# Performance work log

Hardware: AMD Instinct MI355X
Metric: run time of the kernel (lower is better)

## Reference

```python
import jax, jax.numpy as jnp
import numpy as np


def setup_inputs() -> dict:
    key = jax.random.key(0)
    k_x, k_q, k_k, k_v = jax.random.split(key, 4)
    B, S, D = 8, 1024, 768
    H, DH = 12, 64
    scale = 1.0 / np.sqrt(D)
    return {
        "x": jax.random.normal(k_x, (B, S, D), dtype=jnp.float32),
        "Wq": jax.random.normal(k_q, (H, D, DH), dtype=jnp.float32) * scale,
        "Wk": jax.random.normal(k_k, (H, D, DH), dtype=jnp.float32) * scale,
        "Wv": jax.random.normal(k_v, (H, D, DH), dtype=jnp.float32) * scale,
    }


def reference(x, Wq, Wk, Wv):
    # x: [B, S, D]; Wq/Wk/Wv: [H, D, DH] (per-head Linear weights, no bias)
    B, S, D = x.shape
    H, _, DH = Wq.shape
    q = jnp.einsum("bsd,hde->bhse", x, Wq)  # [B,H,S,DH]
    k = jnp.einsum("bsd,hde->bhse", x, Wk)
    v = jnp.einsum("bsd,hde->bhse", x, Wv)
    scores = jnp.einsum("bhse,bhte->bhst", q, k) / jnp.sqrt(jnp.float32(DH))
    causal = jnp.tril(jnp.ones((S, S), dtype=bool))  # keep lower triangle
    scores = jnp.where(causal, scores, -jnp.inf)
    attn = jax.nn.softmax(scores, axis=-1)  # dropout = 0.0 -> identity
    ctx = jnp.einsum("bhst,bhte->bhse", attn, v)  # [B,H,S,DH]
    # concat heads on last dim: [B,S,H*DH]
    return ctx.transpose(0, 2, 1, 3).reshape(B, S, H * DH)
```

## Files before the change

kernel.cpp:

```cpp
#include <hip/hip_runtime.h>


#define Bq 8
#define Sq 1024
#define Dq 768
#define Hq 12
#define DHq 64

typedef _Float16 f16;
typedef f16 f16x8 __attribute__((ext_vector_type(8)));
typedef float f32x4 __attribute__((ext_vector_type(4)));

#define MFMA16(a, b, c) __builtin_amdgcn_mfma_f32_16x16x32_f16(a, b, c, 0, 0, 0)

#define QSCL 0.1803368801111244f

#if __has_builtin(__builtin_amdgcn_exp2f)
#define EXP2(x) __builtin_amdgcn_exp2f(x)
#else
#define EXP2(x) exp2f(x)
#endif

__device__ __forceinline__ void gload16(const f16* g, f16* l) {
  __builtin_amdgcn_global_load_lds(
      (const __attribute__((address_space(1))) void*)g,
      (__attribute__((address_space(3))) void*)l, 16, 0, 0);
}

__global__ __launch_bounds__(256) void cvt_x_kernel(const float* __restrict__ x,
                                                    f16* __restrict__ xh) {
  int i = blockIdx.x * 256 + threadIdx.x;
  const float4* src = reinterpret_cast<const float4*>(x) + i * 2;
  float4 a = src[0], b = src[1];
  f16x8 o;
  o[0] = (f16)a.x; o[1] = (f16)a.y; o[2] = (f16)a.z; o[3] = (f16)a.w;
  o[4] = (f16)b.x; o[5] = (f16)b.y; o[6] = (f16)b.z; o[7] = (f16)b.w;
  *reinterpret_cast<f16x8*>(xh + i * 8) = o;
}

__global__ __launch_bounds__(256) void cvt_w_kernel(const float* __restrict__ Wq,
                                                    const float* __restrict__ Wk,
                                                    const float* __restrict__ Wv,
                                                    f16* __restrict__ WT) {
  __shared__ float tile[64][65];
  const int kt = blockIdx.x, h = blockIdx.y, w = blockIdx.z;
  const float* W = (w == 0) ? Wq : (w == 1) ? Wk : Wv;
  const int t = threadIdx.x;
  const int c0 = t & 63, r4 = t >> 6;
#pragma unroll
  for (int i = 0; i < 16; i++) {
    int kr = i * 4 + r4;
    tile[kr][c0] = W[((size_t)h * Dq + kt * 64 + kr) * DHq + c0];
  }
  __syncthreads();
#pragma unroll
  for (int i = 0; i < 16; i++) {
    int e2 = i * 4 + r4;
    WT[((size_t)(w * Hq + h) * DHq + e2) * Dq + kt * 64 + c0] = (f16)tile[c0][e2];
  }
}

__global__ __launch_bounds__(256) void proj_kernel(const f16* __restrict__ xh,
                                                   const f16* __restrict__ WT,
                                                   f16* __restrict__ Q,
                                                   f16* __restrict__ K,
                                                   f16* __restrict__ Vt) {
  __shared__ __align__(1024) f16 smem[30720];

  const int L = blockIdx.x;
  const int j = L >> 3;
  const int mt = (L & 7) + 8 * (j & 7);
  const int h = j >> 3;
  const int row0 = mt * 128;
  const int t = threadIdx.x;
  const int wv = t >> 6;
  const int lane = t & 63;
  const int g = lane >> 4;
  const int ql = lane & 15;
  const int wvm = wv >> 1, wvn = wv & 1;

  const int lr = lane >> 2;
  const int scg = (lane & 3) ^ ((lane >> 3) & 3);

  const f16* xsrc = xh + (size_t)row0 * Dq;
  const f16* wsrc = WT + (size_t)h * DHq * Dq;

  const f16* gA0 = xsrc + (size_t)(wv * 32 + lr) * Dq + scg * 8;
  const f16* gA1 = gA0 + (size_t)16 * Dq;
  const int n0 = wv * 48 + lr, n1 = n0 + 16, n2 = n0 + 32;
  const f16* gB0 = wsrc + ((size_t)(n0 >> 6) * Hq * DHq + (n0 & 63)) * Dq + scg * 8;
  const f16* gB1 = wsrc + ((size_t)(n1 >> 6) * Hq * DHq + (n1 & 63)) * Dq + scg * 8;
  const f16* gB2 = wsrc + ((size_t)(n2 >> 6) * Hq * DHq + (n2 & 63)) * Dq + scg * 8;

  f32x4 acc[4][6] = {};

#define PROJ_STAGE(buf)                                              \
  do {                                                               \
    f16* sA_ = smem + (buf) * 4096 + wv * 1024;                      \
    f16* sB_ = smem + 12288 + (buf) * 6144 + wv * 1536;              \
    gload16(gA0, sA_); gload16(gA1, sA_ + 512);                      \
    gload16(gB0, sB_); gload16(gB1, sB_ + 512);                      \
    gload16(gB2, sB_ + 1024);                                        \
    gA0 += 32; gA1 += 32; gB0 += 32; gB1 += 32; gB2 += 32;           \
  } while (0)

  PROJ_STAGE(0);
  PROJ_STAGE(1);

  const int rq = (g ^ ((ql >> 1) & 3)) * 8;
  const f16* rA = smem + (wvm * 64 + ql) * 32 + rq;
  const f16* rB = smem + 12288 + (wvn * 96 + ql) * 32 + rq;

#pragma unroll
  for (int step = 0; step < 24; step++) {
    if (step < 23) asm volatile("s_waitcnt vmcnt(5) lgkmcnt(0)" ::: "memory");
    else           asm volatile("s_waitcnt vmcnt(0) lgkmcnt(0)" ::: "memory");
    __builtin_amdgcn_s_barrier();
    __builtin_amdgcn_sched_barrier(0);
    if (step < 22) PROJ_STAGE((step + 2) % 3);
    const int cur = step % 3;
    f16x8 af[4], bf[6];
#pragma unroll
    for (int mf = 0; mf < 4; mf++)
      af[mf] = *reinterpret_cast<const f16x8*>(rA + cur * 4096 + mf * 512);
#pragma unroll
    for (int nf = 0; nf < 6; nf++)
      bf[nf] = *reinterpret_cast<const f16x8*>(rB + cur * 6144 + nf * 512);
    __builtin_amdgcn_s_setprio(1);
#pragma unroll
    for (int mf = 0; mf < 4; mf++)
#pragma unroll
      for (int nf = 0; nf < 6; nf++)
        acc[mf][nf] = MFMA16(af[mf], bf[nf], acc[mf][nf]);
    __builtin_amdgcn_s_setprio(0);
  }
#undef PROJ_STAGE
  __syncthreads();

  const int b = row0 >> 10;
  const int s0 = row0 & 1023;
  const size_t base_sd = ((size_t)(b * Hq + h) * Sq) * DHq;

#pragma unroll
  for (int nf = 0; nf < 6; nf++) {
    const int c = wvn * 96 + nf * 16 + ql;
    const int w = c >> 6;
    if (w < 2) {
      f16* dst = (w == 0 ? Q : K);
      const float scl = (w == 0) ? QSCL : 1.0f;
      const int e = c & 63;
#pragma unroll
      for (int mf = 0; mf < 4; mf++) {
        const int sr = wvm * 64 + mf * 16 + g * 4;
#pragma unroll
        for (int r = 0; r < 4; r++)
          dst[base_sd + (size_t)(s0 + sr + r) * DHq + e] = (f16)(acc[mf][nf][r] * scl);
      }
    }
  }

  f16* vbuf = smem;
#pragma unroll
  for (int nf = 2; nf < 6; nf++) {
    if (wvn == 1) {
      const int e = (96 + nf * 16 + ql) & 63;
#pragma unroll
      for (int mf = 0; mf < 4; mf++) {
        const int sr = wvm * 64 + mf * 16 + g * 4;
        union { f16 hh[4]; uint2 u; } z;
#pragma unroll
        for (int r = 0; r < 4; r++) z.hh[r] = (f16)acc[mf][nf][r];
        *reinterpret_cast<uint2*>(&vbuf[e * 136 + sr]) = z.u;
      }
    }
  }
  __syncthreads();
#pragma unroll
  for (int i = 0; i < 4; i++) {
    int c = t + 256 * i;
    int e = c >> 4, p = (c & 15) * 8;
    *reinterpret_cast<uint4*>(Vt + base_sd + (size_t)e * Sq + s0 + p) =
        *reinterpret_cast<const uint4*>(vbuf + e * 136 + p);
  }
}

__global__ __launch_bounds__(256) void attn_kernel(const f16* __restrict__ Q,
                                                   const f16* __restrict__ K,
                                                   const f16* __restrict__ Vt,
                                                   float* __restrict__ out) {
  __shared__ __align__(16) f16 k_lds[2][64][72];
  __shared__ __align__(16) f16 vt_lds[2][64][72];
  __shared__ __align__(16) f16 p_lds[4][16][72];

  const int L = blockIdx.x;
  const int i = L >> 3;
  const int bh = (L & 7) * Hq + (i % Hq);
  const int p = 7 - (i / Hq);
  const int MT = 2 * p + 1;
  const int t = threadIdx.x;
  const int wv = t >> 6;
  const int lane = t & 63;
  const int g = lane >> 4;
  const int ql = lane & 15;

  const f16* Qb = Q + (size_t)bh * Sq * DHq;
  const f16* Kb = K + (size_t)bh * Sq * DHq;
  const f16* Vtb = Vt + (size_t)bh * DHq * Sq;
  const int b = bh / Hq, h = bh % Hq;

  const int r0 = t >> 3;
  const int p0 = (t & 7) * 8;

  const int qg0 = 2 * p * 64 + wv * 16 + ql;
  const int qg1 = qg0 + 64;
  f16x8 qf[2][2];
  qf[0][0] = *reinterpret_cast<const f16x8*>(Qb + (size_t)qg0 * DHq + g * 8);
  qf[0][1] = *reinterpret_cast<const f16x8*>(Qb + (size_t)qg0 * DHq + 32 + g * 8);
  qf[1][0] = *reinterpret_cast<const f16x8*>(Qb + (size_t)qg1 * DHq + g * 8);
  qf[1][1] = *reinterpret_cast<const f16x8*>(Qb + (size_t)qg1 * DHq + 32 + g * 8);

  f32x4 o_acc[2][4] = {};
  float m_r[2] = { -__builtin_inff(), -__builtin_inff() };
  float l_r[2] = { 0.f, 0.f };

  uint4 kreg0, kreg1, vreg0, vreg1;
  kreg0 = *reinterpret_cast<const uint4*>(Kb + (size_t)r0 * DHq + p0);
  kreg1 = *reinterpret_cast<const uint4*>(Kb + (size_t)(32 + r0) * DHq + p0);
  vreg0 = *reinterpret_cast<const uint4*>(Vtb + (size_t)r0 * Sq + p0);
  vreg1 = *reinterpret_cast<const uint4*>(Vtb + (size_t)(32 + r0) * Sq + p0);
  *reinterpret_cast<uint4*>(&k_lds[0][r0][p0]) = kreg0;
  *reinterpret_cast<uint4*>(&k_lds[0][32 + r0][p0]) = kreg1;
  *reinterpret_cast<uint4*>(&vt_lds[0][r0][p0]) = vreg0;
  *reinterpret_cast<uint4*>(&vt_lds[0][32 + r0][p0]) = vreg1;
  kreg0 = *reinterpret_cast<const uint4*>(Kb + (size_t)(64 + r0) * DHq + p0);
  kreg1 = *reinterpret_cast<const uint4*>(Kb + (size_t)(96 + r0) * DHq + p0);
  vreg0 = *reinterpret_cast<const uint4*>(Vtb + (size_t)r0 * Sq + 64 + p0);
  vreg1 = *reinterpret_cast<const uint4*>(Vtb + (size_t)(32 + r0) * Sq + 64 + p0);
  __syncthreads();

  int cur = 0;
  for (int kt = 0; kt <= MT; kt++) {
    if (kt < MT) {
      *reinterpret_cast<uint4*>(&k_lds[cur ^ 1][r0][p0]) = kreg0;
      *reinterpret_cast<uint4*>(&k_lds[cur ^ 1][32 + r0][p0]) = kreg1;
      *reinterpret_cast<uint4*>(&vt_lds[cur ^ 1][r0][p0]) = vreg0;
      *reinterpret_cast<uint4*>(&vt_lds[cur ^ 1][32 + r0][p0]) = vreg1;
      if (kt + 2 <= MT) {
        const int kv0 = (kt + 2) * 64;
        kreg0 = *reinterpret_cast<const uint4*>(Kb + (size_t)(kv0 + r0) * DHq + p0);
        kreg1 = *reinterpret_cast<const uint4*>(Kb + (size_t)(kv0 + 32 + r0) * DHq + p0);
        vreg0 = *reinterpret_cast<const uint4*>(Vtb + (size_t)r0 * Sq + kv0 + p0);
        vreg1 = *reinterpret_cast<const uint4*>(Vtb + (size_t)(32 + r0) * Sq + kv0 + p0);
      }
    }

    f16x8 kf[4][2], vf[4][2];
#pragma unroll
    for (int nt = 0; nt < 4; nt++) {
      kf[nt][0] = *reinterpret_cast<const f16x8*>(&k_lds[cur][nt * 16 + ql][g * 8]);
      kf[nt][1] = *reinterpret_cast<const f16x8*>(&k_lds[cur][nt * 16 + ql][32 + g * 8]);
      vf[nt][0] = *reinterpret_cast<const f16x8*>(&vt_lds[cur][nt * 16 + ql][g * 8]);
      vf[nt][1] = *reinterpret_cast<const f16x8*>(&vt_lds[cur][nt * 16 + ql][32 + g * 8]);
    }

#pragma unroll
    for (int qs = 0; qs < 2; qs++) {
      if (qs == 0 && kt > 2 * p) continue;
      f32x4 sf[4] = {};
      __builtin_amdgcn_s_setprio(1);
#pragma unroll
      for (int nt = 0; nt < 4; nt++) {
        sf[nt] = MFMA16(kf[nt][0], qf[qs][0], sf[nt]);
        sf[nt] = MFMA16(kf[nt][1], qf[qs][1], sf[nt]);
      }
      __builtin_amdgcn_s_setprio(0);

      if (kt == 2 * p + qs) {
#pragma unroll
        for (int nt = 0; nt < 4; nt++)
#pragma unroll
          for (int r = 0; r < 4; r++)
            if (nt * 16 + g * 4 + r > wv * 16 + ql) sf[nt][r] = -__builtin_inff();
      }

      float t0 = fmaxf(fmaxf(sf[0][0], sf[0][1]), fmaxf(sf[0][2], sf[0][3]));
      float t1 = fmaxf(fmaxf(sf[1][0], sf[1][1]), fmaxf(sf[1][2], sf[1][3]));
      float t2 = fmaxf(fmaxf(sf[2][0], sf[2][1]), fmaxf(sf[2][2], sf[2][3]));
      float t3 = fmaxf(fmaxf(sf[3][0], sf[3][1]), fmaxf(sf[3][2], sf[3][3]));
      float lm = fmaxf(fmaxf(t0, t1), fmaxf(t2, t3));

      if (!__all(lm <= m_r[qs] + 8.f)) {
        float rowmax = fmaxf(lm, __shfl_xor(lm, 16, 64));
        rowmax = fmaxf(rowmax, __shfl_xor(rowmax, 32, 64));
        float mnew = fmaxf(m_r[qs], rowmax);
        float corr = EXP2(m_r[qs] - mnew);
        l_r[qs] *= corr;
#pragma unroll
        for (int nt = 0; nt < 4; nt++) {
          o_acc[qs][nt][0] *= corr; o_acc[qs][nt][1] *= corr;
          o_acc[qs][nt][2] *= corr; o_acc[qs][nt][3] *= corr;
        }
        m_r[qs] = mnew;
      }

      float pv[4][4];
#pragma unroll
      for (int nt = 0; nt < 4; nt++)
#pragma unroll
        for (int r = 0; r < 4; r++) pv[nt][r] = EXP2(sf[nt][r] - m_r[qs]);
      float s0 = (pv[0][0] + pv[0][1]) + (pv[0][2] + pv[0][3]);
      float s1 = (pv[1][0] + pv[1][1]) + (pv[1][2] + pv[1][3]);
      float s2 = (pv[2][0] + pv[2][1]) + (pv[2][2] + pv[2][3]);
      float s3 = (pv[3][0] + pv[3][1]) + (pv[3][2] + pv[3][3]);
      l_r[qs] += (s0 + s1) + (s2 + s3);

#pragma unroll
      for (int nt = 0; nt < 4; nt++) {
        union { f16 hh[4]; uint2 u; } z;
        z.hh[0] = (f16)pv[nt][0]; z.hh[1] = (f16)pv[nt][1];
        z.hh[2] = (f16)pv[nt][2]; z.hh[3] = (f16)pv[nt][3];
        *reinterpret_cast<uint2*>(&p_lds[wv][ql][nt * 16 + g * 4]) = z.u;
      }
      f16x8 pf[2];
      pf[0] = *reinterpret_cast<const f16x8*>(&p_lds[wv][ql][g * 8]);
      pf[1] = *reinterpret_cast<const f16x8*>(&p_lds[wv][ql][32 + g * 8]);

      __builtin_amdgcn_s_setprio(1);
#pragma unroll
      for (int nt = 0; nt < 4; nt++) {
        o_acc[qs][nt] = MFMA16(vf[nt][0], pf[0], o_acc[qs][nt]);
        o_acc[qs][nt] = MFMA16(vf[nt][1], pf[1], o_acc[qs][nt]);
      }
      __builtin_amdgcn_s_setprio(0);
    }

    __syncthreads();
    cur ^= 1;
  }

#pragma unroll
  for (int qs = 0; qs < 2; qs++) {
    const int qg = qs ? qg1 : qg0;
    float lt = l_r[qs];
    lt += __shfl_xor(lt, 16, 64);
    lt += __shfl_xor(lt, 32, 64);
    float rl = 1.0f / lt;
    float* op = out + ((size_t)(b * Sq + qg)) * (Hq * DHq) + h * DHq;
#pragma unroll
    for (int nt = 0; nt < 4; nt++) {
      float4 st = { o_acc[qs][nt][0] * rl, o_acc[qs][nt][1] * rl,
                    o_acc[qs][nt][2] * rl, o_acc[qs][nt][3] * rl };
      *reinterpret_cast<float4*>(op + nt * 16 + g * 4) = st;
    }
  }
}

extern "C" void kernel_launch(void* const* d_in, const int* in_sizes, int n_in,
                              void* d_out, int out_size, void* d_ws, size_t ws_size,
                              hipStream_t stream) {
  const float* x = (const float*)d_in[0];
  const float* Wq = (const float*)d_in[1];
  const float* Wk = (const float*)d_in[2];
  const float* Wv = (const float*)d_in[3];
  float* out = (float*)d_out;

  const size_t off_xb = 0;
  const size_t off_wt = 12582912;
  const size_t off_q = 16121856;
  const size_t off_k = 28704768;
  const size_t off_v = 41287680;
  const size_t need = 53870592;
  if (ws_size < need) return;

  char* ws = (char*)d_ws;
  f16* xh = (f16*)(ws + off_xb);
  f16* WT = (f16*)(ws + off_wt);
  f16* Qd = (f16*)(ws + off_q);
  f16* Kd = (f16*)(ws + off_k);
  f16* Vtd = (f16*)(ws + off_v);

  cvt_x_kernel<<<3072, 256, 0, stream>>>(x, xh);
  cvt_w_kernel<<<dim3(12, 12, 3), 256, 0, stream>>>(Wq, Wk, Wv, WT);
  proj_kernel<<<768, 256, 0, stream>>>(xh, WT, Qd, Kd, Vtd);
  attn_kernel<<<768, 256, 0, stream>>>(Qd, Kd, Vtd, out);
}
```

Baseline: 81.74 us.

## Double projection M-tile to 256 rows per block to reuse weight tiles

The QKV projection kernel now computes 256 rows per block instead of 128. Each wave holds two accumulator sets that share the same B-fragment loads, so each weight tile is read once per two A halves and the grid halves to 384 blocks. Shared memory, registers and the pipeline wait count grow to match, and launch bounds are set to one block per CU. The risks are much higher register pressure and fewer blocks for 256 CUs, which could hurt occupancy and tail balance.

```diff
diff --git a/kernel.cpp b/kernel.cpp
--- a/kernel.cpp
+++ b/kernel.cpp
@@ -60,18 +60,17 @@
   }
 }
 
-__global__ __launch_bounds__(256) void proj_kernel(const f16* __restrict__ xh,
-                                                   const f16* __restrict__ WT,
-                                                   f16* __restrict__ Q,
-                                                   f16* __restrict__ K,
-                                                   f16* __restrict__ Vt) {
-  __shared__ __align__(1024) f16 smem[30720];
+__global__ __launch_bounds__(256, 1) void proj_kernel(const f16* __restrict__ xh,
+                                                      const f16* __restrict__ WT,
+                                                      f16* __restrict__ Q,
+                                                      f16* __restrict__ K,
+                                                      f16* __restrict__ Vt) {
+  __shared__ __align__(1024) f16 smem[43008];
 
   const int L = blockIdx.x;
-  const int j = L >> 3;
-  const int mt = (L & 7) + 8 * (j & 7);
-  const int h = j >> 3;
-  const int row0 = mt * 128;
+  const int mt = L & 31;
+  const int h = L >> 5;
+  const int row0 = mt * 256;
   const int t = threadIdx.x;
   const int wv = t >> 6;
   const int lane = t & 63;
@@ -85,23 +84,28 @@
   const f16* xsrc = xh + (size_t)row0 * Dq;
   const f16* wsrc = WT + (size_t)h * DHq * Dq;
 
-  const f16* gA0 = xsrc + (size_t)(wv * 32 + lr) * Dq + scg * 8;
+  const f16* gA0 = xsrc + (size_t)(wv * 64 + lr) * Dq + scg * 8;
   const f16* gA1 = gA0 + (size_t)16 * Dq;
+  const f16* gA2 = gA0 + (size_t)32 * Dq;
+  const f16* gA3 = gA0 + (size_t)48 * Dq;
   const int n0 = wv * 48 + lr, n1 = n0 + 16, n2 = n0 + 32;
   const f16* gB0 = wsrc + ((size_t)(n0 >> 6) * Hq * DHq + (n0 & 63)) * Dq + scg * 8;
   const f16* gB1 = wsrc + ((size_t)(n1 >> 6) * Hq * DHq + (n1 & 63)) * Dq + scg * 8;
   const f16* gB2 = wsrc + ((size_t)(n2 >> 6) * Hq * DHq + (n2 & 63)) * Dq + scg * 8;
 
-  f32x4 acc[4][6] = {};
+  f32x4 acc0[4][6] = {};
+  f32x4 acc1[4][6] = {};
 
 #define PROJ_STAGE(buf)                                              \
   do {                                                               \
-    f16* sA_ = smem + (buf) * 4096 + wv * 1024;                      \
-    f16* sB_ = smem + 12288 + (buf) * 6144 + wv * 1536;              \
-    gload16(gA0, sA_); gload16(gA1, sA_ + 512);                      \
+    f16* sA_ = smem + (buf) * 8192 + wv * 2048;                      \
+    f16* sB_ = smem + 24576 + (buf) * 6144 + wv * 1536;              \
+    gload16(gA0, sA_);        gload16(gA1, sA_ + 512);               \
+    gload16(gA2, sA_ + 1024); gload16(gA3, sA_ + 1536);              \
     gload16(gB0, sB_); gload16(gB1, sB_ + 512);                      \
     gload16(gB2, sB_ + 1024);                                        \
-    gA0 += 32; gA1 += 32; gB0 += 32; gB1 += 32; gB2 += 32;           \
+    gA0 += 32; gA1 += 32; gA2 += 32; gA3 += 32;                      \
+    gB0 += 32; gB1 += 32; gB2 += 32;                                 \
   } while (0)
 
   PROJ_STAGE(0);
@@ -109,29 +113,37 @@
 
   const int rq = (g ^ ((ql >> 1) & 3)) * 8;
   const f16* rA = smem + (wvm * 64 + ql) * 32 + rq;
-  const f16* rB = smem + 12288 + (wvn * 96 + ql) * 32 + rq;
+  const f16* rB = smem + 24576 + (wvn * 96 + ql) * 32 + rq;
 
 #pragma unroll
   for (int step = 0; step < 24; step++) {
-    if (step < 23) asm volatile("s_waitcnt vmcnt(5) lgkmcnt(0)" ::: "memory");
+    if (step < 23) asm volatile("s_waitcnt vmcnt(7) lgkmcnt(0)" ::: "memory");
     else           asm volatile("s_waitcnt vmcnt(0) lgkmcnt(0)" ::: "memory");
     __builtin_amdgcn_s_barrier();
     __builtin_amdgcn_sched_barrier(0);
     if (step < 22) PROJ_STAGE((step + 2) % 3);
     const int cur = step % 3;
-    f16x8 af[4], bf[6];
-#pragma unroll
-    for (int mf = 0; mf < 4; mf++)
-      af[mf] = *reinterpret_cast<const f16x8*>(rA + cur * 4096 + mf * 512);
+    f16x8 bf[6];
 #pragma unroll
     for (int nf = 0; nf < 6; nf++)
       bf[nf] = *reinterpret_cast<const f16x8*>(rB + cur * 6144 + nf * 512);
+    f16x8 af0[4], af1[4];
+#pragma unroll
+    for (int mf = 0; mf < 4; mf++) {
+      af0[mf] = *reinterpret_cast<const f16x8*>(rA + cur * 8192 + mf * 512);
+      af1[mf] = *reinterpret_cast<const f16x8*>(rA + cur * 8192 + 4096 + mf * 512);
+    }
     __builtin_amdgcn_s_setprio(1);
 #pragma unroll
     for (int mf = 0; mf < 4; mf++)
 #pragma unroll
       for (int nf = 0; nf < 6; nf++)
-        acc[mf][nf] = MFMA16(af[mf], bf[nf], acc[mf][nf]);
+        acc0[mf][nf] = MFMA16(af0[mf], bf[nf], acc0[mf][nf]);
+#pragma unroll
+    for (int mf = 0; mf < 4; mf++)
+#pragma unroll
+      for (int nf = 0; nf < 6; nf++)
+        acc1[mf][nf] = MFMA16(af1[mf], bf[nf], acc1[mf][nf]);
     __builtin_amdgcn_s_setprio(0);
   }
 #undef PROJ_STAGE
@@ -142,45 +154,53 @@
   const size_t base_sd = ((size_t)(b * Hq + h) * Sq) * DHq;
 
 #pragma unroll
-  for (int nf = 0; nf < 6; nf++) {
-    const int c = wvn * 96 + nf * 16 + ql;
-    const int w = c >> 6;
-    if (w < 2) {
-      f16* dst = (w == 0 ? Q : K);
-      const float scl = (w == 0) ? QSCL : 1.0f;
-      const int e = c & 63;
-#pragma unroll
-      for (int mf = 0; mf < 4; mf++) {
-        const int sr = wvm * 64 + mf * 16 + g * 4;
-#pragma unroll
-        for (int r = 0; r < 4; r++)
-          dst[base_sd + (size_t)(s0 + sr + r) * DHq + e] = (f16)(acc[mf][nf][r] * scl);
+  for (int mh = 0; mh < 2; mh++) {
+#pragma unroll
+    for (int nf = 0; nf < 6; nf++) {
+      const int c = wvn * 96 + nf * 16 + ql;
+      const int w = c >> 6;
+      if (w < 2) {
+        f16* dst = (w == 0 ? Q : K);
+        const float scl = (w == 0) ? QSCL : 1.0f;
+        const int e = c & 63;
+#pragma unroll
+        for (int mf = 0; mf < 4; mf++) {
+          const int sr = mh * 128 + wvm * 64 + mf * 16 + g * 4;
+          const f32x4& a = mh ? acc1[mf][nf] : acc0[mf][nf];
+#pragma unroll
+          for (int r = 0; r < 4; r++)
+            dst[base_sd + (size_t)(s0 + sr + r) * DHq + e] = (f16)(a[r] * scl);
+        }
       }
     }
   }
 
   f16* vbuf = smem;
 #pragma unroll
-  for (int nf = 2; nf < 6; nf++) {
-    if (wvn == 1) {
-      const int e = (96 + nf * 16 + ql) & 63;
-#pragma unroll
-      for (int mf = 0; mf < 4; mf++) {
-        const int sr = wvm * 64 + mf * 16 + g * 4;
-        union { f16 hh[4]; uint2 u; } z;
-#pragma unroll
-        for (int r = 0; r < 4; r++) z.hh[r] = (f16)acc[mf][nf][r];
-        *reinterpret_cast<uint2*>(&vbuf[e * 136 + sr]) = z.u;
+  for (int mh = 0; mh < 2; mh++) {
+#pragma unroll
+    for (int nf = 2; nf < 6; nf++) {
+      if (wvn == 1) {
+        const int e = nf * 16 + ql - 32;
+#pragma unroll
+        for (int mf = 0; mf < 4; mf++) {
+          const int sr = mh * 128 + wvm * 64 + mf * 16 + g * 4;
+          const f32x4& a = mh ? acc1[mf][nf] : acc0[mf][nf];
+          union { f16 hh[4]; uint2 u; } z;
+#pragma unroll
+          for (int r = 0; r < 4; r++) z.hh[r] = (f16)a[r];
+          *reinterpret_cast<uint2*>(&vbuf[e * 264 + sr]) = z.u;
+        }
       }
     }
   }
   __syncthreads();
 #pragma unroll
-  for (int i = 0; i < 4; i++) {
+  for (int i = 0; i < 8; i++) {
     int c = t + 256 * i;
-    int e = c >> 4, p = (c & 15) * 8;
+    int e = c >> 5, p = (c & 31) * 8;
     *reinterpret_cast<uint4*>(Vt + base_sd + (size_t)e * Sq + s0 + p) =
-        *reinterpret_cast<const uint4*>(vbuf + e * 136 + p);
+        *reinterpret_cast<const uint4*>(vbuf + e * 264 + p);
   }
 }
 
@@ -381,6 +401,6 @@
 
   cvt_x_kernel<<<3072, 256, 0, stream>>>(x, xh);
   cvt_w_kernel<<<dim3(12, 12, 3), 256, 0, stream>>>(Wq, Wk, Wv, WT);
-  proj_kernel<<<768, 256, 0, stream>>>(xh, WT, Qd, Kd, Vtd);
+  proj_kernel<<<384, 256, 0, stream>>>(xh, WT, Qd, Kd, Vtd);
   attn_kernel<<<768, 256, 0, stream>>>(Qd, Kd, Vtd, out);
 }
```

New measurement: 85.76 us. 1.05x slower.

## Load A operand directly from global into registers, shrink LDS for two blocks

Applied to the files above, without the earlier changes.

In the projection kernel, the x (A) tiles are no longer staged through LDS. Each wave loads its A fragments straight from global memory into registers, double-buffered between even and odd steps, while only the weight (B) tiles keep the triple-buffered LDS pipeline. This cuts shared memory from 60KB to 36KB and adds a launch bound of 2 blocks per CU, aiming for higher occupancy and less LDS traffic. In exchange, the A loads are replicated across the two N-waves and are less coalesced, and register pressure rises, which could force spilling under the 2-block bound.

```diff
diff --git a/kernel.cpp b/kernel.cpp
--- a/kernel.cpp
+++ b/kernel.cpp
@@ -60,12 +60,12 @@
   }
 }
 
-__global__ __launch_bounds__(256) void proj_kernel(const f16* __restrict__ xh,
-                                                   const f16* __restrict__ WT,
-                                                   f16* __restrict__ Q,
-                                                   f16* __restrict__ K,
-                                                   f16* __restrict__ Vt) {
-  __shared__ __align__(1024) f16 smem[30720];
+__global__ __launch_bounds__(256, 2) void proj_kernel(const f16* __restrict__ xh,
+                                                      const f16* __restrict__ WT,
+                                                      f16* __restrict__ Q,
+                                                      f16* __restrict__ K,
+                                                      f16* __restrict__ Vt) {
+  __shared__ __align__(1024) f16 smem[18432];
 
   const int L = blockIdx.x;
   const int j = L >> 3;
@@ -85,56 +85,77 @@
   const f16* xsrc = xh + (size_t)row0 * Dq;
   const f16* wsrc = WT + (size_t)h * DHq * Dq;
 
-  const f16* gA0 = xsrc + (size_t)(wv * 32 + lr) * Dq + scg * 8;
-  const f16* gA1 = gA0 + (size_t)16 * Dq;
+  const f16* aP0 = xsrc + (size_t)(wvm * 64 + ql) * Dq + g * 8;
+  const f16* aP1 = aP0 + (size_t)16 * Dq;
+  const f16* aP2 = aP0 + (size_t)32 * Dq;
+  const f16* aP3 = aP0 + (size_t)48 * Dq;
+
   const int n0 = wv * 48 + lr, n1 = n0 + 16, n2 = n0 + 32;
   const f16* gB0 = wsrc + ((size_t)(n0 >> 6) * Hq * DHq + (n0 & 63)) * Dq + scg * 8;
   const f16* gB1 = wsrc + ((size_t)(n1 >> 6) * Hq * DHq + (n1 & 63)) * Dq + scg * 8;
   const f16* gB2 = wsrc + ((size_t)(n2 >> 6) * Hq * DHq + (n2 & 63)) * Dq + scg * 8;
 
   f32x4 acc[4][6] = {};
-
-#define PROJ_STAGE(buf)                                              \
+  uint4 arE[4], arO[4];
+
+#define B_STAGE(buf)                                                 \
   do {                                                               \
-    f16* sA_ = smem + (buf) * 4096 + wv * 1024;                      \
-    f16* sB_ = smem + 12288 + (buf) * 6144 + wv * 1536;              \
-    gload16(gA0, sA_); gload16(gA1, sA_ + 512);                      \
+    f16* sB_ = smem + (buf) * 6144 + wv * 1536;                      \
     gload16(gB0, sB_); gload16(gB1, sB_ + 512);                      \
     gload16(gB2, sB_ + 1024);                                        \
-    gA0 += 32; gA1 += 32; gB0 += 32; gB1 += 32; gB2 += 32;           \
+    gB0 += 32; gB1 += 32; gB2 += 32;                                 \
   } while (0)
 
-  PROJ_STAGE(0);
-  PROJ_STAGE(1);
+#define A_LOAD(dst)                                                  \
+  do {                                                               \
+    dst[0] = *reinterpret_cast<const uint4*>(aP0);                   \
+    dst[1] = *reinterpret_cast<const uint4*>(aP1);                   \
+    dst[2] = *reinterpret_cast<const uint4*>(aP2);                   \
+    dst[3] = *reinterpret_cast<const uint4*>(aP3);                   \
+    aP0 += 32; aP1 += 32; aP2 += 32; aP3 += 32;                      \
+  } while (0)
+
+  B_STAGE(0);
+  A_LOAD(arE);
+  B_STAGE(1);
 
   const int rq = (g ^ ((ql >> 1) & 3)) * 8;
-  const f16* rA = smem + (wvm * 64 + ql) * 32 + rq;
-  const f16* rB = smem + 12288 + (wvn * 96 + ql) * 32 + rq;
+  const f16* rB = smem + (wvn * 96 + ql) * 32 + rq;
 
 #pragma unroll
   for (int step = 0; step < 24; step++) {
-    if (step < 23) asm volatile("s_waitcnt vmcnt(5) lgkmcnt(0)" ::: "memory");
+    if (step < 23) asm volatile("s_waitcnt vmcnt(3) lgkmcnt(0)" ::: "memory");
     else           asm volatile("s_waitcnt vmcnt(0) lgkmcnt(0)" ::: "memory");
     __builtin_amdgcn_s_barrier();
     __builtin_amdgcn_sched_barrier(0);
-    if (step < 22) PROJ_STAGE((step + 2) % 3);
+    if (step < 23) {
+      if ((step + 1) & 1) A_LOAD(arO);
+      else                A_LOAD(arE);
+    }
+    if (step < 22) B_STAGE((step + 2) % 3);
     const int cur = step % 3;
-    f16x8 af[4], bf[6];
-#pragma unroll
-    for (int mf = 0; mf < 4; mf++)
-      af[mf] = *reinterpret_cast<const f16x8*>(rA + cur * 4096 + mf * 512);
+    f16x8 bf[6];
 #pragma unroll
     for (int nf = 0; nf < 6; nf++)
       bf[nf] = *reinterpret_cast<const f16x8*>(rB + cur * 6144 + nf * 512);
+    const uint4* arc = (step & 1) ? arO : arE;
     __builtin_amdgcn_s_setprio(1);
 #pragma unroll
-    for (int mf = 0; mf < 4; mf++)
+    for (int mf = 0; mf < 4; mf++) {
+      f16x8 af;
+      {
+        union { uint4 u; f16x8 v; } z;
+        z.u = arc[mf];
+        af = z.v;
+      }
 #pragma unroll
       for (int nf = 0; nf < 6; nf++)
-        acc[mf][nf] = MFMA16(af[mf], bf[nf], acc[mf][nf]);
+        acc[mf][nf] = MFMA16(af, bf[nf], acc[mf][nf]);
+    }
     __builtin_amdgcn_s_setprio(0);
   }
-#undef PROJ_STAGE
+#undef B_STAGE
+#undef A_LOAD
   __syncthreads();
 
   const int b = row0 >> 10;
```

Measured after the change: 100.3 us. +22.7%, slower.
